# Optimization experiments

Hardware: AMD Instinct MI355X
Metric: run time of the kernel (lower is better)

## Reference

```python
import jax, jax.numpy as jnp
import numpy as np

STATE_DIM = 128
NUM_STATES = 16
BATCH = 16384


def setup_inputs() -> dict:
    key = jax.random.key(0)
    k1, k2, k3, k4 = jax.random.split(key, 4)
    x = jax.random.normal(k1, (BATCH, STATE_DIM), dtype=jnp.float32)
    state_idx = jax.random.randint(k2, (BATCH,), 0, NUM_STATES)
    A_all = jax.random.normal(k3, (NUM_STATES, STATE_DIM, STATE_DIM), dtype=jnp.float32)
    C_all = jax.random.normal(k4, (NUM_STATES, STATE_DIM, STATE_DIM), dtype=jnp.float32)
    return {"x": x, "state_idx": state_idx, "A_all": A_all, "C_all": C_all}


def reference(x, state_idx, A_all, C_all):
    # Per-sample expert matrix gather: [B, D, D]
    Ag = A_all[state_idx]
    Cg = C_all[state_idx]
    # state = relu(x @ A_i) per sample, batched via einsum
    state = jax.nn.relu(jnp.einsum('bd,bde->be', x, Ag))
    # observation = state @ C_i
    out = jnp.einsum('be,bef->bf', state, Cg)
    return out
```

## Files before the change

### kernel.cpp

```cpp
#include <hip/hip_runtime.h>

#define D 128
#define NS 16
#define BATCH 16384
#define TILE 64
#define CHUNK 512

typedef __attribute__((ext_vector_type(8))) short short8;
typedef __attribute__((ext_vector_type(4))) float f32x4;

__device__ __forceinline__ unsigned short f2bf(float f) {
  unsigned u = __builtin_bit_cast(unsigned, f);
  u += 0x7FFFu + ((u >> 16) & 1u);
  return (unsigned short)(u >> 16);
}

__device__ __forceinline__ uint4 pack8(float4 a, float4 b) {
  unsigned short p[8];
  p[0] = f2bf(a.x); p[1] = f2bf(a.y); p[2] = f2bf(a.z); p[3] = f2bf(a.w);
  p[4] = f2bf(b.x); p[5] = f2bf(b.y); p[6] = f2bf(b.z); p[7] = f2bf(b.w);
  return *(const uint4*)p;
}

__global__ __launch_bounds__(512, 4) void ssm_fused(
    const float* __restrict__ x,
    const int* __restrict__ sidx,
    const float* __restrict__ A_all,
    const float* __restrict__ C_all,
    float* __restrict__ out) {
  __shared__ unsigned short XH[TILE * D];
  __shared__ int rowlist[CHUNK];
  __shared__ int wcnt[8];

  const int b = blockIdx.x;
  const int s = (b & 7) | (((b >> 3) & 1) << 3);
  const int c0 = (b >> 4) * CHUNK;
  const int tid = threadIdx.x;
  const int lane = tid & 63, w = tid >> 6;
  const int l15 = lane & 15, quad = lane >> 4;

  const int v0 = sidx[c0 + tid];

  short8 aW[4], cW[4];
  {
    const size_t wb = (size_t)s * D * D;
    const int col = w * 16 + l15;
#pragma unroll
    for (int kb = 0; kb < 4; kb++) {
      const float* pA = A_all + wb + (size_t)(kb * 32 + quad * 8) * D + col;
      const float* pC = C_all + wb + (size_t)(kb * 32 + quad * 8) * D + col;
      unsigned short ta[8], tc[8];
#pragma unroll
      for (int j = 0; j < 8; j++) {
        ta[j] = f2bf(pA[j * D]);
        tc[j] = f2bf(pC[j * D]);
      }
      aW[kb] = *(const short8*)ta;
      cW[kb] = *(const short8*)tc;
    }
  }

  const unsigned long long lanelt = (1ull << lane) - 1ull;
  const unsigned long long m0 = __ballot(v0 == s);
  if (lane == 0) wcnt[w] = (int)__popcll(m0);
  __syncthreads();
  int pre = 0, cnt = 0;
#pragma unroll
  for (int ww = 0; ww < 8; ww++) {
    const int c = wcnt[ww];
    if (ww < w) pre += c;
    cnt += c;
  }
  if (v0 == s) rowlist[pre + (int)__popcll(m0 & lanelt)] = c0 + tid;
  if (cnt == 0) return;

#pragma unroll 1
  for (int i0 = 0; i0 < cnt; i0 += TILE) {
    __syncthreads();

    {
      const int r = tid >> 3, q8 = tid & 7;
      const int rid = (i0 + r < cnt) ? rowlist[i0 + r] : -1;
      const int cA = q8 * 2, cB = q8 * 2 + 1;
      uint4* dA = (uint4*)&XH[r * D + ((cA ^ (r & 15)) << 3)];
      uint4* dB = (uint4*)&XH[r * D + ((cB ^ (r & 15)) << 3)];
      if (rid >= 0) {
        const float4* src = (const float4*)(x + (size_t)rid * D + q8 * 16);
        *dA = pack8(src[0], src[1]);
        *dB = pack8(src[2], src[3]);
      } else {
        uint4 z = {0, 0, 0, 0};
        *dA = z;
        *dB = z;
      }
    }
    __syncthreads();

    f32x4 acc[4];
#pragma unroll
    for (int ti = 0; ti < 4; ti++) acc[ti] = (f32x4){0.f, 0.f, 0.f, 0.f};
#pragma unroll
    for (int kb = 0; kb < 4; kb++) {
      short8 aF[4];
#pragma unroll
      for (int ti = 0; ti < 4; ti++)
        aF[ti] = *(const short8*)&XH[(ti * 16 + l15) * D +
                                     (((kb * 4 + quad) ^ l15) << 3)];
#pragma unroll
      for (int ti = 0; ti < 4; ti++)
        acc[ti] = __builtin_amdgcn_mfma_f32_16x16x32_bf16(aF[ti], aW[kb],
                                                          acc[ti], 0, 0, 0);
    }
    __syncthreads();

#pragma unroll
    for (int ti = 0; ti < 4; ti++)
#pragma unroll
      for (int rr = 0; rr < 4; rr++) {
        float v = acc[ti][rr];
        const int row = ti * 16 + quad * 4 + rr;
        const int ch = (w * 2 + (l15 >> 3)) ^ (quad * 4 + rr);
        XH[row * D + (ch << 3) + (l15 & 7)] = f2bf(v > 0.f ? v : 0.f);
      }
    __syncthreads();

#pragma unroll
    for (int ti = 0; ti < 4; ti++) acc[ti] = (f32x4){0.f, 0.f, 0.f, 0.f};
#pragma unroll
    for (int kb = 0; kb < 4; kb++) {
      short8 aF[4];
#pragma unroll
      for (int ti = 0; ti < 4; ti++)
        aF[ti] = *(const short8*)&XH[(ti * 16 + l15) * D +
                                     (((kb * 4 + quad) ^ l15) << 3)];
#pragma unroll
      for (int ti = 0; ti < 4; ti++)
        acc[ti] = __builtin_amdgcn_mfma_f32_16x16x32_bf16(aF[ti], cW[kb],
                                                          acc[ti], 0, 0, 0);
    }

#pragma unroll
    for (int ti = 0; ti < 4; ti++)
#pragma unroll
      for (int rr = 0; rr < 4; rr++) {
        const int rl = i0 + ti * 16 + quad * 4 + rr;
        if (rl < cnt) {
          out[(size_t)rowlist[rl] * D + w * 16 + l15] = acc[ti][rr];
        }
      }
  }
}

extern "C" void kernel_launch(void* const* d_in, const int* in_sizes, int n_in,
                              void* d_out, int out_size, void* d_ws, size_t ws_size,
                              hipStream_t stream) {
  const float* x = (const float*)d_in[0];
  const int* sidx = (const int*)d_in[1];
  const float* A_all = (const float*)d_in[2];
  const float* C_all = (const float*)d_in[3];
  float* out = (float*)d_out;

  ssm_fused<<<BATCH / CHUNK * NS, 512, 0, stream>>>(x, sidx, A_all, C_all, out);
}
```

Baseline: 71.65 us.

## Double chunk size per block and skip empty 16-row MFMA subtiles

Each block now scans 1024 batch rows instead of 512, so half as many blocks are launched and each block converts its per-state A and C weights to bf16 only half as often. Launch bounds drop to 2 blocks per SM. Inside the tile loop, 16-row subtiles beyond the valid row count skip their LDS loads, MFMAs, ReLU writeback and stores, which avoids MFMA work on the partly empty last tile. The costs are fewer blocks for latency hiding and uniform branches around the MFMA sequence.

```diff
diff --git a/kernel.cpp b/kernel.cpp
--- a/kernel.cpp
+++ b/kernel.cpp
@@ -4,7 +4,7 @@
 #define NS 16
 #define BATCH 16384
 #define TILE 64
-#define CHUNK 512
+#define CHUNK 1024
 
 typedef __attribute__((ext_vector_type(8))) short short8;
 typedef __attribute__((ext_vector_type(4))) float f32x4;
@@ -22,7 +22,7 @@
   return *(const uint4*)p;
 }
 
-__global__ __launch_bounds__(512, 4) void ssm_fused(
+__global__ __launch_bounds__(512, 2) void ssm_fused(
     const float* __restrict__ x,
     const int* __restrict__ sidx,
     const float* __restrict__ A_all,
@@ -30,7 +30,7 @@
     float* __restrict__ out) {
   __shared__ unsigned short XH[TILE * D];
   __shared__ int rowlist[CHUNK];
-  __shared__ int wcnt[8];
+  __shared__ int wcnt[16];
 
   const int b = blockIdx.x;
   const int s = (b & 7) | (((b >> 3) & 1) << 3);
@@ -40,6 +40,7 @@
   const int l15 = lane & 15, quad = lane >> 4;
 
   const int v0 = sidx[c0 + tid];
+  const int v1 = sidx[c0 + 512 + tid];
 
   short8 aW[4], cW[4];
   {
@@ -62,21 +63,25 @@
 
   const unsigned long long lanelt = (1ull << lane) - 1ull;
   const unsigned long long m0 = __ballot(v0 == s);
-  if (lane == 0) wcnt[w] = (int)__popcll(m0);
+  const unsigned long long m1 = __ballot(v1 == s);
+  if (lane == 0) { wcnt[w] = (int)__popcll(m0); wcnt[8 + w] = (int)__popcll(m1); }
   __syncthreads();
-  int pre = 0, cnt = 0;
+  int pre0 = 0, pre1 = 0, tot0 = 0, cnt = 0;
 #pragma unroll
   for (int ww = 0; ww < 8; ww++) {
-    const int c = wcnt[ww];
-    if (ww < w) pre += c;
-    cnt += c;
+    if (ww < w) { pre0 += wcnt[ww]; pre1 += wcnt[8 + ww]; }
+    tot0 += wcnt[ww];
+    cnt += wcnt[ww] + wcnt[8 + ww];
   }
-  if (v0 == s) rowlist[pre + (int)__popcll(m0 & lanelt)] = c0 + tid;
+  if (v0 == s) rowlist[pre0 + (int)__popcll(m0 & lanelt)] = c0 + tid;
+  if (v1 == s) rowlist[tot0 + pre1 + (int)__popcll(m1 & lanelt)] = c0 + 512 + tid;
   if (cnt == 0) return;
 
 #pragma unroll 1
   for (int i0 = 0; i0 < cnt; i0 += TILE) {
     __syncthreads();
+
+    const bool tv1 = (i0 + 16 < cnt), tv2 = (i0 + 32 < cnt), tv3 = (i0 + 48 < cnt);
 
     {
       const int r = tid >> 3, q8 = tid & 7;
@@ -103,18 +108,29 @@
     for (int kb = 0; kb < 4; kb++) {
       short8 aF[4];
 #pragma unroll
-      for (int ti = 0; ti < 4; ti++)
+      for (int ti = 0; ti < 4; ti++) {
+        if (ti == 1 && !tv1) continue;
+        if (ti == 2 && !tv2) continue;
+        if (ti == 3 && !tv3) continue;
         aF[ti] = *(const short8*)&XH[(ti * 16 + l15) * D +
                                      (((kb * 4 + quad) ^ l15) << 3)];
+      }
 #pragma unroll
-      for (int ti = 0; ti < 4; ti++)
+      for (int ti = 0; ti < 4; ti++) {
+        if (ti == 1 && !tv1) continue;
+        if (ti == 2 && !tv2) continue;
+        if (ti == 3 && !tv3) continue;
         acc[ti] = __builtin_amdgcn_mfma_f32_16x16x32_bf16(aF[ti], aW[kb],
                                                           acc[ti], 0, 0, 0);
+      }
     }
     __syncthreads();
 
 #pragma unroll
-    for (int ti = 0; ti < 4; ti++)
+    for (int ti = 0; ti < 4; ti++) {
+      if (ti == 1 && !tv1) continue;
+      if (ti == 2 && !tv2) continue;
+      if (ti == 3 && !tv3) continue;
 #pragma unroll
       for (int rr = 0; rr < 4; rr++) {
         float v = acc[ti][rr];
@@ -122,6 +138,7 @@
         const int ch = (w * 2 + (l15 >> 3)) ^ (quad * 4 + rr);
         XH[row * D + (ch << 3) + (l15 & 7)] = f2bf(v > 0.f ? v : 0.f);
       }
+    }
     __syncthreads();
 
 #pragma unroll
@@ -130,17 +147,28 @@
     for (int kb = 0; kb < 4; kb++) {
       short8 aF[4];
 #pragma unroll
-      for (int ti = 0; ti < 4; ti++)
+      for (int ti = 0; ti < 4; ti++) {
+        if (ti == 1 && !tv1) continue;
+        if (ti == 2 && !tv2) continue;
+        if (ti == 3 && !tv3) continue;
         aF[ti] = *(const short8*)&XH[(ti * 16 + l15) * D +
                                      (((kb * 4 + quad) ^ l15) << 3)];
+      }
 #pragma unroll
-      for (int ti = 0; ti < 4; ti++)
+      for (int ti = 0; ti < 4; ti++) {
+        if (ti == 1 && !tv1) continue;
+        if (ti == 2 && !tv2) continue;
+        if (ti == 3 && !tv3) continue;
         acc[ti] = __builtin_amdgcn_mfma_f32_16x16x32_bf16(aF[ti], cW[kb],
                                                           acc[ti], 0, 0, 0);
+      }
     }
 
 #pragma unroll
-    for (int ti = 0; ti < 4; ti++)
+    for (int ti = 0; ti < 4; ti++) {
+      if (ti == 1 && !tv1) continue;
+      if (ti == 2 && !tv2) continue;
+      if (ti == 3 && !tv3) continue;
 #pragma unroll
       for (int rr = 0; rr < 4; rr++) {
         const int rl = i0 + ti * 16 + quad * 4 + rr;
@@ -148,6 +176,7 @@
           out[(size_t)rowlist[rl] * D + w * 16 + l15] = acc[ti][rr];
         }
       }
+    }
   }
 }
 
```

After: 73.14 us. 1.02x slower.
